# Optimization experiments

Hardware: AMD Instinct MI355X
Metric: run time of the kernel (lower is better)

Reference implementation:

```python
import jax, jax.numpy as jnp
import numpy as np

I_SIZE, H_SIZE, O_SIZE = 3, 128, 3
B, T, A = 512, 50, 64


def _xavier(k, shape):
    fan_out, fan_in = shape
    limit = float(np.sqrt(6.0 / (fan_in + fan_out)))
    return jax.random.uniform(k, shape, minval=-limit, maxval=limit, dtype=jnp.float32)


def setup_inputs() -> dict:
    key = jax.random.key(0)
    ks = jax.random.split(key, 6)
    src = jax.random.normal(ks[0], (B, T, A * I_SIZE), dtype=jnp.float32)
    return {
        "src": src,
        "W_ih_enc": _xavier(ks[1], (H_SIZE, I_SIZE)),
        "W_hh_enc": _xavier(ks[2], (H_SIZE, H_SIZE)),
        "b_ih_enc": jnp.zeros((H_SIZE,), jnp.float32),
        "b_hh_enc": jnp.zeros((H_SIZE,), jnp.float32),
        "W_ih_dec": _xavier(ks[3], (H_SIZE, O_SIZE)),
        "W_hh_dec": _xavier(ks[4], (H_SIZE, H_SIZE)),
        "b_ih_dec": jnp.zeros((H_SIZE,), jnp.float32),
        "b_hh_dec": jnp.zeros((H_SIZE,), jnp.float32),
        "fc_W": _xavier(ks[5], (O_SIZE, H_SIZE)),
        "fc_b": jnp.zeros((O_SIZE,), jnp.float32),
        "pred_len": 12,
    }


def reference(src, W_ih_enc, W_hh_enc, b_ih_enc, b_hh_enc,
              W_ih_dec, W_hh_dec, b_ih_dec, b_hh_dec, fc_W, fc_b, pred_len):
    b, t, f = src.shape
    a = f // I_SIZE
    # (b, t, a*I) -> (t, b*a, I): agents batched together (vectorizes the per-agent loop)
    xs = src.reshape(b, t, a, I_SIZE).transpose(1, 0, 2, 3).reshape(t, b * a, I_SIZE)

    def enc_step(h, x_t):
        h = jnp.tanh(x_t @ W_ih_enc.T + b_ih_enc + h @ W_hh_enc.T + b_hh_enc)
        return h, None

    h0 = jnp.zeros((b * a, H_SIZE), src.dtype)
    h_enc, _ = jax.lax.scan(enc_step, h0, xs)

    # decoder input = last observed position of each agent
    dec_in0 = xs[-1]  # (b*a, I)

    def dec_step(carry, _):
        h, inp = carry
        h = jnp.tanh(inp @ W_ih_dec.T + b_ih_dec + h @ W_hh_dec.T + b_hh_dec)
        pred = h @ fc_W.T + fc_b  # (b*a, O)
        return (h, pred), pred

    _, preds = jax.lax.scan(dec_step, (h_enc, dec_in0), None, length=pred_len)
    # (pred_len, b*a, O) -> (b, pred_len, a*O)
    out = preds.reshape(pred_len, b, a, O_SIZE).transpose(1, 0, 2, 3).reshape(b, pred_len, a * O_SIZE)
    return out
```

## Files before the change

kernel.cpp:

```cpp
#include <hip/hip_runtime.h>
#include <stdint.h>

typedef _Float16 f16x8 __attribute__((ext_vector_type(8)));
typedef float f32x4 __attribute__((ext_vector_type(4)));
typedef unsigned int u32x4 __attribute__((ext_vector_type(4)));

#define T_OBS 50
#define PRED 12

#define DEC_OFF 20480
#define FC_OFF  40960
#define WS_ELEMS 43008

__device__ __forceinline__ int unperm(int k) {
  return (k & 3) | (((k >> 3) & 3) << 2) | (((k >> 2) & 1) << 4) | (k & 0x60);
}

__global__ void prep_kernel(const float* __restrict__ Wih_e, const float* __restrict__ Whh_e,
                            const float* __restrict__ bih_e, const float* __restrict__ bhh_e,
                            const float* __restrict__ Wih_d, const float* __restrict__ Whh_d,
                            const float* __restrict__ bih_d, const float* __restrict__ bhh_d,
                            const float* __restrict__ fcW,
                            unsigned short* __restrict__ ws) {
  int idx = blockIdx.x * 256 + threadIdx.x;
  if (idx >= WS_ELEMS) return;
  float val = 0.0f;
  if (idx < FC_OFF) {
    const bool enc = idx < DEC_OFF;
    const int e = enc ? idx : idx - DEC_OFF;
    const int j = e & 7;
    const int lane = (e >> 3) & 63;
    const int rem = e >> 9;
    const int kt = rem % 5;
    const int t = rem / 5;
    const int n = 16 * t + (lane & 15);
    const int kappa = 32 * kt + ((lane >> 4) << 3) + j;
    const float* Wih = enc ? Wih_e : Wih_d;
    const float* Whh = enc ? Whh_e : Whh_d;
    const float* bih = enc ? bih_e : bih_d;
    const float* bhh = enc ? bhh_e : bhh_d;
    if (kappa < 128)       val = Whh[n * 128 + unperm(kappa)];
    else if (kappa < 131)  val = Wih[n * 3 + (kappa - 128)];
    else if (kappa == 131) val = bih[n] + bhh[n];
  } else {
    const int e = idx - FC_OFF;
    const int j = e & 7;
    const int lane = (e >> 3) & 63;
    const int kt = e >> 9;
    const int o = lane & 15;
    const int kappa = 32 * kt + ((lane >> 4) << 3) + j;
    if (o < 3) val = fcW[o * 128 + unperm(kappa)];
  }
  _Float16 h = (_Float16)val;
  ws[idx] = __builtin_bit_cast(unsigned short, h);
}

__device__ __forceinline__ float tanh_fast(float v) {
  float e = __builtin_amdgcn_exp2f(v * 2.8853900817779268f);
  return __builtin_fmaf(-2.0f, __builtin_amdgcn_rcpf(1.0f + e), 1.0f);
}

__device__ __forceinline__ unsigned int pk2(float a, float b) {
  return __builtin_bit_cast(unsigned int, __builtin_amdgcn_cvt_pkrtz(a, b));
}

__device__ __forceinline__ f16x8 ldfrag(const unsigned short* p) {
  return __builtin_bit_cast(f16x8, *(const u32x4*)p);
}

__device__ __forceinline__ f16x8 mkxf(float a, float b, float c) {
  u32x4 u;
  u[0] = pk2(a, b);
  u[1] = pk2(c, 1.0f);
  u[2] = 0u;
  u[3] = 0u;
  return __builtin_bit_cast(f16x8, u);
}

__global__ __launch_bounds__(256, 1) void traj_kernel(
    const float* __restrict__ src, const unsigned short* __restrict__ ws,
    const float* __restrict__ fcb, float* __restrict__ out) {
  const int lane = (int)(threadIdx.x & 63u);
  const int w = (int)(threadIdx.x >> 6u);
  const int sX = blockIdx.x * 128 + w * 32 + (lane & 15);
  const int sY = sX + 16;
  const float* xpX = src + (size_t)(sX >> 6) * (T_OBS * 192) + (sX & 63) * 3;
  const float* xpY = src + (size_t)(sY >> 6) * (T_OBS * 192) + (sY & 63) * 3;

  f16x8 A[40];
  #pragma unroll
  for (int i = 0; i < 40; ++i)
    A[i] = ldfrag(ws + (size_t)(i * 64 + lane) * 8);

  f16x8 BfX[4], BfY[4];
  #pragma unroll
  for (int i = 0; i < 4; ++i) {
    u32x4 zz = (u32x4)0u;
    BfX[i] = __builtin_bit_cast(f16x8, zz);
    BfY[i] = __builtin_bit_cast(f16x8, zz);
  }
  f16x8 xfX = mkxf(xpX[0], xpX[1], xpX[2]);
  f16x8 xfY = mkxf(xpY[0], xpY[1], xpY[2]);

  const f32x4 z = (f32x4){0.f, 0.f, 0.f, 0.f};
  f32x4 aX[8], aY[8];

  auto rnn_step = [&]() {
    #pragma unroll
    for (int t = 0; t < 8; ++t) {
      aX[t] = __builtin_amdgcn_mfma_f32_16x16x32_f16(A[t * 5 + 4], xfX, z, 0, 0, 0);
      #pragma unroll
      for (int kt = 0; kt < 4; ++kt)
        aX[t] = __builtin_amdgcn_mfma_f32_16x16x32_f16(A[t * 5 + kt], BfX[kt], aX[t], 0, 0, 0);
    }
    #pragma unroll
    for (int t = 0; t < 8; ++t) {
      aY[t] = __builtin_amdgcn_mfma_f32_16x16x32_f16(A[t * 5 + 4], xfY, z, 0, 0, 0);
      #pragma unroll
      for (int kt = 0; kt < 4; ++kt)
        aY[t] = __builtin_amdgcn_mfma_f32_16x16x32_f16(A[t * 5 + kt], BfY[kt], aY[t], 0, 0, 0);
    }
    #pragma unroll
    for (int kt = 0; kt < 4; ++kt) {
      u32x4 F;
      F[0] = pk2(tanh_fast(aX[2 * kt][0]),     tanh_fast(aX[2 * kt][1]));
      F[1] = pk2(tanh_fast(aX[2 * kt][2]),     tanh_fast(aX[2 * kt][3]));
      F[2] = pk2(tanh_fast(aX[2 * kt + 1][0]), tanh_fast(aX[2 * kt + 1][1]));
      F[3] = pk2(tanh_fast(aX[2 * kt + 1][2]), tanh_fast(aX[2 * kt + 1][3]));
      BfX[kt] = __builtin_bit_cast(f16x8, F);
    }
    #pragma unroll
    for (int kt = 0; kt < 4; ++kt) {
      u32x4 F;
      F[0] = pk2(tanh_fast(aY[2 * kt][0]),     tanh_fast(aY[2 * kt][1]));
      F[1] = pk2(tanh_fast(aY[2 * kt][2]),     tanh_fast(aY[2 * kt][3]));
      F[2] = pk2(tanh_fast(aY[2 * kt + 1][0]), tanh_fast(aY[2 * kt + 1][1]));
      F[3] = pk2(tanh_fast(aY[2 * kt + 1][2]), tanh_fast(aY[2 * kt + 1][3]));
      BfY[kt] = __builtin_bit_cast(f16x8, F);
    }
  };

  for (int s = 0; s < T_OBS; ++s) {
    const int t2 = (s < T_OBS - 1) ? s + 1 : s;
    const float nX0 = xpX[t2 * 192], nX1 = xpX[t2 * 192 + 1], nX2 = xpX[t2 * 192 + 2];
    const float nY0 = xpY[t2 * 192], nY1 = xpY[t2 * 192 + 1], nY2 = xpY[t2 * 192 + 2];
    rnn_step();
    xfX = mkxf(nX0, nX1, nX2);
    xfY = mkxf(nY0, nY1, nY2);
  }

  #pragma unroll
  for (int i = 0; i < 40; ++i)
    A[i] = ldfrag(ws + DEC_OFF + (size_t)(i * 64 + lane) * 8);
  f16x8 Afc[4];
  #pragma unroll
  for (int kt = 0; kt < 4; ++kt)
    Afc[kt] = ldfrag(ws + FC_OFF + (size_t)(kt * 64 + lane) * 8);
  const float fb0 = fcb[0], fb1 = fcb[1], fb2 = fcb[2];

  float* opX = out + (size_t)(sX >> 6) * (PRED * 192) + (sX & 63) * 3;
  float* opY = out + (size_t)(sY >> 6) * (PRED * 192) + (sY & 63) * 3;

  for (int p = 0; p < PRED; ++p) {
    rnn_step();
    f32x4 pX = __builtin_amdgcn_mfma_f32_16x16x32_f16(Afc[0], BfX[0], z, 0, 0, 0);
    f32x4 pY = __builtin_amdgcn_mfma_f32_16x16x32_f16(Afc[0], BfY[0], z, 0, 0, 0);
    #pragma unroll
    for (int kt = 1; kt < 4; ++kt) {
      pX = __builtin_amdgcn_mfma_f32_16x16x32_f16(Afc[kt], BfX[kt], pX, 0, 0, 0);
      pY = __builtin_amdgcn_mfma_f32_16x16x32_f16(Afc[kt], BfY[kt], pY, 0, 0, 0);
    }
    const float pX0 = pX[0] + fb0, pX1 = pX[1] + fb1, pX2 = pX[2] + fb2;
    const float pY0 = pY[0] + fb0, pY1 = pY[1] + fb1, pY2 = pY[2] + fb2;
    if (lane < 16) {
      opX[p * 192 + 0] = pX0; opX[p * 192 + 1] = pX1; opX[p * 192 + 2] = pX2;
      opY[p * 192 + 0] = pY0; opY[p * 192 + 1] = pY1; opY[p * 192 + 2] = pY2;
    }
    xfX = mkxf(pX0, pX1, pX2);
    xfY = mkxf(pY0, pY1, pY2);
  }
}

extern "C" void kernel_launch(void* const* d_in, const int* in_sizes, int n_in,
                              void* d_out, int out_size, void* d_ws, size_t ws_size,
                              hipStream_t stream) {
  const float* src   = (const float*)d_in[0];
  const float* Wih_e = (const float*)d_in[1];
  const float* Whh_e = (const float*)d_in[2];
  const float* bih_e = (const float*)d_in[3];
  const float* bhh_e = (const float*)d_in[4];
  const float* Wih_d = (const float*)d_in[5];
  const float* Whh_d = (const float*)d_in[6];
  const float* bih_d = (const float*)d_in[7];
  const float* bhh_d = (const float*)d_in[8];
  const float* fcW   = (const float*)d_in[9];
  const float* fcb   = (const float*)d_in[10];
  (void)in_sizes; (void)n_in; (void)out_size; (void)ws_size;

  unsigned short* ws = (unsigned short*)d_ws;

  prep_kernel<<<(WS_ELEMS + 255) / 256, 256, 0, stream>>>(
      Wih_e, Whh_e, bih_e, bhh_e, Wih_d, Whh_d, bih_d, bhh_d, fcW, ws);

  traj_kernel<<<256, 256, 0, stream>>>(src, ws, fcb, (float*)d_out);
}
```

Measured before the change: 104.9 us.

## Software-pipeline X/Y sequence halves to overlap MFMA with tanh VALU work

```diff
diff --git a/kernel.cpp b/kernel.cpp
--- a/kernel.cpp
+++ b/kernel.cpp
@@ -77,6 +77,21 @@
   return __builtin_bit_cast(f16x8, u);
 }
 
+__device__ __forceinline__ void sgb_mix40() {
+  #pragma unroll
+  for (int i = 0; i < 40; ++i) {
+    __builtin_amdgcn_sched_group_barrier(0x008, 1, 0);
+    __builtin_amdgcn_sched_group_barrier(0x002, 4, 0);
+  }
+}
+__device__ __forceinline__ void sgb_mix44() {
+  #pragma unroll
+  for (int i = 0; i < 44; ++i) {
+    __builtin_amdgcn_sched_group_barrier(0x008, 1, 0);
+    __builtin_amdgcn_sched_group_barrier(0x002, 4, 0);
+  }
+}
+
 __global__ __launch_bounds__(256, 1) void traj_kernel(
     const float* __restrict__ src, const unsigned short* __restrict__ ws,
     const float* __restrict__ fcb, float* __restrict__ out) {
@@ -105,7 +120,7 @@
   const f32x4 z = (f32x4){0.f, 0.f, 0.f, 0.f};
   f32x4 aX[8], aY[8];
 
-  auto rnn_step = [&]() {
+  auto MFMA_X = [&]() {
     #pragma unroll
     for (int t = 0; t < 8; ++t) {
       aX[t] = __builtin_amdgcn_mfma_f32_16x16x32_f16(A[t * 5 + 4], xfX, z, 0, 0, 0);
@@ -113,6 +128,8 @@
       for (int kt = 0; kt < 4; ++kt)
         aX[t] = __builtin_amdgcn_mfma_f32_16x16x32_f16(A[t * 5 + kt], BfX[kt], aX[t], 0, 0, 0);
     }
+  };
+  auto MFMA_Y = [&]() {
     #pragma unroll
     for (int t = 0; t < 8; ++t) {
       aY[t] = __builtin_amdgcn_mfma_f32_16x16x32_f16(A[t * 5 + 4], xfY, z, 0, 0, 0);
@@ -120,6 +137,8 @@
       for (int kt = 0; kt < 4; ++kt)
         aY[t] = __builtin_amdgcn_mfma_f32_16x16x32_f16(A[t * 5 + kt], BfY[kt], aY[t], 0, 0, 0);
     }
+  };
+  auto TANH_X = [&]() {
     #pragma unroll
     for (int kt = 0; kt < 4; ++kt) {
       u32x4 F;
@@ -129,6 +148,8 @@
       F[3] = pk2(tanh_fast(aX[2 * kt + 1][2]), tanh_fast(aX[2 * kt + 1][3]));
       BfX[kt] = __builtin_bit_cast(f16x8, F);
     }
+  };
+  auto TANH_Y = [&]() {
     #pragma unroll
     for (int kt = 0; kt < 4; ++kt) {
       u32x4 F;
@@ -140,14 +161,23 @@
     }
   };
 
-  for (int s = 0; s < T_OBS; ++s) {
-    const int t2 = (s < T_OBS - 1) ? s + 1 : s;
-    const float nX0 = xpX[t2 * 192], nX1 = xpX[t2 * 192 + 1], nX2 = xpX[t2 * 192 + 2];
-    const float nY0 = xpY[t2 * 192], nY1 = xpY[t2 * 192 + 1], nY2 = xpY[t2 * 192 + 2];
-    rnn_step();
+  MFMA_X();
+  for (int s = 0; s < T_OBS - 1; ++s) {
+    const float nX0 = xpX[(s + 1) * 192], nX1 = xpX[(s + 1) * 192 + 1], nX2 = xpX[(s + 1) * 192 + 2];
+    MFMA_Y();
+    TANH_X();
     xfX = mkxf(nX0, nX1, nX2);
+    sgb_mix40();
+    const float nY0 = xpY[(s + 1) * 192], nY1 = xpY[(s + 1) * 192 + 1], nY2 = xpY[(s + 1) * 192 + 2];
+    MFMA_X();
+    TANH_Y();
     xfY = mkxf(nY0, nY1, nY2);
-  }
+    sgb_mix40();
+  }
+  MFMA_Y();
+  TANH_X();
+  sgb_mix40();
+  TANH_Y();
 
   #pragma unroll
   for (int i = 0; i < 40; ++i)
@@ -162,22 +192,27 @@
   float* opY = out + (size_t)(sY >> 6) * (PRED * 192) + (sY & 63) * 3;
 
   for (int p = 0; p < PRED; ++p) {
-    rnn_step();
+    MFMA_X();
+    MFMA_Y();
+    TANH_X();
     f32x4 pX = __builtin_amdgcn_mfma_f32_16x16x32_f16(Afc[0], BfX[0], z, 0, 0, 0);
+    #pragma unroll
+    for (int kt = 1; kt < 4; ++kt)
+      pX = __builtin_amdgcn_mfma_f32_16x16x32_f16(Afc[kt], BfX[kt], pX, 0, 0, 0);
+    const float pX0 = pX[0] + fb0, pX1 = pX[1] + fb1, pX2 = pX[2] + fb2;
+    xfX = mkxf(pX0, pX1, pX2);
+    sgb_mix44();
+    TANH_Y();
     f32x4 pY = __builtin_amdgcn_mfma_f32_16x16x32_f16(Afc[0], BfY[0], z, 0, 0, 0);
     #pragma unroll
-    for (int kt = 1; kt < 4; ++kt) {
-      pX = __builtin_amdgcn_mfma_f32_16x16x32_f16(Afc[kt], BfX[kt], pX, 0, 0, 0);
+    for (int kt = 1; kt < 4; ++kt)
       pY = __builtin_amdgcn_mfma_f32_16x16x32_f16(Afc[kt], BfY[kt], pY, 0, 0, 0);
-    }
-    const float pX0 = pX[0] + fb0, pX1 = pX[1] + fb1, pX2 = pX[2] + fb2;
     const float pY0 = pY[0] + fb0, pY1 = pY[1] + fb1, pY2 = pY[2] + fb2;
+    xfY = mkxf(pY0, pY1, pY2);
     if (lane < 16) {
       opX[p * 192 + 0] = pX0; opX[p * 192 + 1] = pX1; opX[p * 192 + 2] = pX2;
       opY[p * 192 + 0] = pY0; opY[p * 192 + 1] = pY1; opY[p * 192 + 2] = pY2;
     }
-    xfX = mkxf(pX0, pX1, pX2);
-    xfY = mkxf(pY0, pY1, pY2);
   }
 }
 
```

Measured after the change: 113.4 us. 8.1% more time.
